# Kernel tuning notes

Hardware: AMD Instinct MI355X
Metric: run time of the kernel (lower is better)

## Reference

```python
import jax, jax.numpy as jnp
import numpy as np

B, T, N, H, D = 4, 512, 4, 8, 64
FACTOR = 5


def setup_inputs() -> dict:
    key = jax.random.key(0)
    k1, k2, k3, k4 = jax.random.split(key, 4)
    queries = jax.random.normal(k1, (B, T, N, H, D), dtype=jnp.float32)
    keys = jax.random.normal(k2, (B, T, N, H, D), dtype=jnp.float32)
    values = jax.random.normal(k3, (B, T, N, H, D), dtype=jnp.float32)
    sample_k = min(FACTOR * int(np.ceil(np.log(T))), T)  # = 35
    index_sample = jax.random.randint(k4, (T, sample_k), 0, T)
    return {"queries": queries, "keys": keys, "values": values,
            "index_sample": index_sample}


def _merge_heads(x):
    # [B, T, N, H, D] -> [B, H, T, N*D]  (matches transpose(3,2).reshape.transpose(2,1))
    b, t, n, h, d = x.shape
    return jnp.transpose(x, (0, 1, 3, 2, 4)).reshape(b, t, h, n * d).transpose(0, 2, 1, 3)


def reference(queries, keys, values, index_sample):
    b, t, n, h, d = queries.shape
    e = n * d
    Q = _merge_heads(queries)   # [B, H, T, E]
    K = _merge_heads(keys)
    V = _merge_heads(values)
    u = index_sample.shape[1]   # sample_k == n_top == factor*ceil(ln T)

    # --- _prob_QK: sampled QK scores, sparsity measure, top-u query select ---
    K_sample = K[:, :, index_sample, :]                      # [B, H, T, u, E]
    QK_sample = jnp.einsum('bhte,bhtse->bhts', Q, K_sample)  # [B, H, T, u]
    M = QK_sample.max(axis=-1) - QK_sample.sum(axis=-1) / t  # [B, H, T]
    _, M_top = jax.lax.top_k(M, u)                           # [B, H, u]
    Q_reduce = jnp.take_along_axis(Q, M_top[..., None], axis=2)  # [B, H, u, E]
    scores = jnp.einsum('bhue,bhte->bhut', Q_reduce, K)      # [B, H, u, T]

    # scale uses 1/sqrt(d_k) of the ORIGINAL query last dim (D), not N*D
    scores = scores * (1.0 / jnp.sqrt(jnp.asarray(d, scores.dtype)))

    # --- initial context (mask_flag=False): mean of V broadcast over T ---
    context = jnp.broadcast_to(V.mean(axis=2, keepdims=True), (b, h, t, e))

    # --- update context at selected query positions ---
    attn = jax.nn.softmax(scores, axis=-1)                   # [B, H, u, T]
    update = jnp.einsum('bhut,bhte->bhue', attn, V)          # [B, H, u, E]
    bi = jnp.arange(b)[:, None, None]
    hi = jnp.arange(h)[None, :, None]
    context = context.at[bi, hi, M_top].set(update)          # scatter-write

    # [B, H, T, E] -> [B, T, N, H, D]
    out = context.transpose(0, 2, 1, 3).reshape(b, t, h, n, d).transpose(0, 1, 3, 2, 4)
    return out
```

## Files before the change

### kernel.cpp

```cpp
#include <hip/hip_runtime.h>
#include <stdint.h>

#define BB 4
#define TT 512
#define NN 4
#define HH 8
#define DD 64
#define EE 256
#define ROWS 2048
#define UPAD 36
#define NCH 8
#define CH 64


__global__ __launch_bounds__(1024)
void vmean_kernel(const float* __restrict__ v, float* __restrict__ vmean) {
    __shared__ float part[4][EE];
    int bh = blockIdx.x;
    int b = bh >> 3, h = bh & 7;
    int e = threadIdx.x & 255;
    int chunk = threadIdx.x >> 8;
    int n = e >> 6, d = e & 63;
    size_t base = (size_t)b * TT * ROWS + (size_t)(n * HH + h) * DD + d;
    float acc = 0.f;
    int t0 = chunk * 128;
    for (int t = t0; t < t0 + 128; ++t)
        acc += v[base + (size_t)t * ROWS];
    part[chunk][e] = acc;
    __syncthreads();
    if (threadIdx.x < EE)
        vmean[bh * EE + threadIdx.x] =
            (part[0][threadIdx.x] + part[1][threadIdx.x] +
             part[2][threadIdx.x] + part[3][threadIdx.x]) * (1.0f / TT);
}

__global__ void fill_kernel(const float* __restrict__ vmean,
                            float* __restrict__ out) {
    size_t tid4 = ((size_t)blockIdx.x * 256 + threadIdx.x) << 2;
    int d = tid4 & 63;
    size_t rest = tid4 >> 6;
    int h = rest & 7;  rest >>= 3;
    int n = rest & 3;  rest >>= 2;
    int b = (int)(rest >> 9);
    int e = (n << 6) + d;
    int bh = (b << 3) + h;
    float4 val = *(const float4*)(vmean + (size_t)bh * EE + e);
    *(float4*)(out + tid4) = val;
}

__global__ void m_kernel(const float* __restrict__ q,
                         const float* __restrict__ k,
                         const int* __restrict__ idx,
                         float* __restrict__ M, int U) {
    int wave = threadIdx.x >> 6, lane = threadIdx.x & 63;
    int r = (blockIdx.x << 2) + wave;
    int t = r & (TT - 1);
    int bh = r >> 9;
    int b = bh >> 3, h = bh & 7;
    int g = lane >> 4, x = lane & 15;
    int n = x >> 2;
    int dbase = ((x & 3) << 4);
    size_t colbase = (size_t)(n * HH + h) * DD + dbase;
    size_t qrow = ((size_t)(b * TT + t)) * ROWS + colbase;
    float4 qv0 = *(const float4*)(q + qrow);
    float4 qv1 = *(const float4*)(q + qrow + 4);
    float4 qv2 = *(const float4*)(q + qrow + 8);
    float4 qv3 = *(const float4*)(q + qrow + 12);
    float mx = -3.4e38f, sm = 0.f;
    int NB = (U + 3) >> 2;
    for (int bs = 0; bs < NB; ++bs) {
        int s = (bs << 2) + g;
        int valid = s < U;
        int sc = valid ? s : (U - 1);
        int kt = idx[t * U + sc] & (TT - 1);
        size_t krow = ((size_t)(b * TT + kt)) * ROWS + colbase;
        float4 kv0 = *(const float4*)(k + krow);
        float4 kv1 = *(const float4*)(k + krow + 4);
        float4 kv2 = *(const float4*)(k + krow + 8);
        float4 kv3 = *(const float4*)(k + krow + 12);
        float dot = qv0.x * kv0.x + qv0.y * kv0.y + qv0.z * kv0.z + qv0.w * kv0.w
                  + qv1.x * kv1.x + qv1.y * kv1.y + qv1.z * kv1.z + qv1.w * kv1.w
                  + qv2.x * kv2.x + qv2.y * kv2.y + qv2.z * kv2.z + qv2.w * kv2.w
                  + qv3.x * kv3.x + qv3.y * kv3.y + qv3.z * kv3.z + qv3.w * kv3.w;
        #pragma unroll
        for (int off = 1; off < 16; off <<= 1)
            dot += __shfl_xor(dot, off, 64);
        if (valid) { mx = fmaxf(mx, dot); sm += dot; }
    }
    mx = fmaxf(mx, __shfl_xor(mx, 16, 64));
    mx = fmaxf(mx, __shfl_xor(mx, 32, 64));
    sm += __shfl_xor(sm, 16, 64);
    sm += __shfl_xor(sm, 32, 64);
    if (lane == 0) M[r] = mx - sm * (1.0f / TT);
}

__global__ void topk_kernel(const float* __restrict__ M,
                            int* __restrict__ Mtop, int U) {
    __shared__ float sM[TT];
    int bh = blockIdx.x;
    int t = threadIdx.x;
    sM[t] = M[bh * TT + t];
    if (t < 64) Mtop[bh * 64 + t] = 0;
    __syncthreads();
    float mv = sM[t];
    int rank = 0;
    for (int i = 0; i < TT; ++i) {
        float o = sM[i];
        rank += (o > mv) || (o == mv && i < t);
    }
    if (rank < U) Mtop[bh * 64 + rank] = t;
}

__global__ __launch_bounds__(256)
void attn_partial(const float* __restrict__ q, const float* __restrict__ k,
                  const float* __restrict__ v, const int* __restrict__ Mtop,
                  float* __restrict__ Opart, float* __restrict__ ml, int U) {
    __shared__ float qs[UPAD * 130];
    __shared__ float Bs[CH * 132];
    __shared__ float S[UPAD * 68];

    int bx = blockIdx.x;
    int bh = bx >> 3, ch = bx & 7;
    int b = bh >> 3, h = bh & 7;
    int tid = threadIdx.x;
    int wv = tid >> 6, l = tid & 63;

    float acc[4][4];
    #pragma unroll
    for (int i = 0; i < 4; ++i)
        #pragma unroll
        for (int j = 0; j < 4; ++j) acc[i][j] = 0.f;

    for (int h2 = 0; h2 < 2; ++h2) {
        int eb = h2 * 128;
        for (int u = wv; u < UPAD; u += 4) {
            int uu = (u < U) ? u : (U - 1);
            int qt = Mtop[bh * 64 + uu] & (TT - 1);
            size_t rowq = ((size_t)(b * TT + qt)) * ROWS;
            #pragma unroll
            for (int j = 0; j < 2; ++j) {
                int e = eb + l + 64 * j;
                qs[u * 130 + l + 64 * j] = q[rowq + (size_t)((e >> 6) * HH + h) * DD + (e & 63)];
            }
        }
        for (int r = wv; r < CH; r += 4) {
            size_t rowk = ((size_t)(b * TT + ch * CH + r)) * ROWS;
            #pragma unroll
            for (int j = 0; j < 2; ++j) {
                int e = eb + l + 64 * j;
                Bs[r * 129 + l + 64 * j] = k[rowk + (size_t)((e >> 6) * HH + h) * DD + (e & 63)];
            }
        }
        __syncthreads();
        if (tid < 144) {
            int ug = tid >> 4, tg = tid & 15;
            int u0 = ug << 2, t0 = tg << 2;
            for (int e = 0; e < 128; ++e) {
                float kx0 = Bs[(t0 + 0) * 129 + e];
                float kx1 = Bs[(t0 + 1) * 129 + e];
                float kx2 = Bs[(t0 + 2) * 129 + e];
                float kx3 = Bs[(t0 + 3) * 129 + e];
                #pragma unroll
                for (int i = 0; i < 4; ++i) {
                    float qv = qs[(u0 + i) * 130 + e];
                    acc[i][0] += qv * kx0;
                    acc[i][1] += qv * kx1;
                    acc[i][2] += qv * kx2;
                    acc[i][3] += qv * kx3;
                }
            }
        }
        __syncthreads();
    }
    if (tid < 144) {
        int ug = tid >> 4, tg = tid & 15;
        int u0 = ug << 2, t0 = tg << 2;
        #pragma unroll
        for (int i = 0; i < 4; ++i)
            #pragma unroll
            for (int j = 0; j < 4; ++j)
                S[(u0 + i) * 68 + t0 + j] = acc[i][j] * 0.125f;
    }
    __syncthreads();

    if (tid < UPAD) {
        float m = -3.4e38f;
        for (int t = 0; t < CH; ++t) m = fmaxf(m, S[tid * 68 + t]);
        float lsum = 0.f;
        for (int t = 0; t < CH; ++t) {
            float p = __expf(S[tid * 68 + t] - m);
            S[tid * 68 + t] = p;
            lsum += p;
        }
        size_t mli = ((size_t)(bh * NCH + ch) * UPAD + tid) * 2;
        ml[mli] = m;
        ml[mli + 1] = lsum;
    }
    __syncthreads();

    int ugp = tid >> 5, el = tid & 31;
    int u0p = ugp * 5;
    for (int vh = 0; vh < 2; ++vh) {
        for (int r = wv; r < CH; r += 4) {
            size_t rowv = ((size_t)(b * TT + ch * CH + r)) * ROWS;
            #pragma unroll
            for (int j = 0; j < 2; ++j) {
                int e = vh * 128 + l + 64 * j;
                Bs[r * 132 + l + 64 * j] = v[rowv + (size_t)((e >> 6) * HH + h) * DD + (e & 63)];
            }
        }
        __syncthreads();
        float4 o[5];
        #pragma unroll
        for (int i = 0; i < 5; ++i) o[i] = make_float4(0.f, 0.f, 0.f, 0.f);
        for (int t = 0; t < CH; ++t) {
            float4 v4 = *(const float4*)&Bs[t * 132 + 4 * el];
            #pragma unroll
            for (int i = 0; i < 5; ++i) {
                int uc = u0p + i; if (uc > 35) uc = 35;
                float p = S[uc * 68 + t];
                o[i].x += p * v4.x; o[i].y += p * v4.y;
                o[i].z += p * v4.z; o[i].w += p * v4.w;
            }
        }
        #pragma unroll
        for (int i = 0; i < 5; ++i) {
            int u = u0p + i;
            if (u < UPAD)
                *(float4*)&Opart[((size_t)(bh * NCH + ch) * UPAD + u) * EE + vh * 128 + 4 * el] = o[i];
        }
        __syncthreads();
    }
}

__global__ void combine_kernel(const float* __restrict__ Opart,
                               const float* __restrict__ ml,
                               const int* __restrict__ Mtop,
                               float* __restrict__ out, int U) {
    int bx = blockIdx.x;
    int bh = bx / U, ui = bx % U;
    int b = bh >> 3, h = bh & 7;
    int el = threadIdx.x;
    float mc[NCH], lc[NCH];
    float gm = -3.4e38f;
    #pragma unroll
    for (int c = 0; c < NCH; ++c) {
        size_t mli = ((size_t)(bh * NCH + c) * UPAD + ui) * 2;
        mc[c] = ml[mli]; lc[c] = ml[mli + 1];
        gm = fmaxf(gm, mc[c]);
    }
    float L = 0.f;
    float fc[NCH];
    #pragma unroll
    for (int c = 0; c < NCH; ++c) { fc[c] = __expf(mc[c] - gm); L += lc[c] * fc[c]; }
    float inv = 1.0f / L;
    float4 a = make_float4(0.f, 0.f, 0.f, 0.f);
    #pragma unroll
    for (int c = 0; c < NCH; ++c) {
        float4 o = *(const float4*)&Opart[((size_t)(bh * NCH + c) * UPAD + ui) * EE + 4 * el];
        a.x += fc[c] * o.x; a.y += fc[c] * o.y;
        a.z += fc[c] * o.z; a.w += fc[c] * o.w;
    }
    int qt = Mtop[bh * 64 + ui] & (TT - 1);
    int e0 = 4 * el, n = el >> 4;
    size_t ooff = ((size_t)(b * TT + qt)) * ROWS + (size_t)(n * HH + h) * DD + (e0 & 63);
    a.x *= inv; a.y *= inv; a.z *= inv; a.w *= inv;
    *(float4*)(out + ooff) = a;
}

__global__ void update_kernel(const float* __restrict__ q,
                              const float* __restrict__ k,
                              const float* __restrict__ v,
                              const int* __restrict__ Mtop,
                              float* __restrict__ out, int U) {
    __shared__ float qs[EE];
    __shared__ float sc[TT];
    __shared__ float red[256];
    int blk = blockIdx.x;
    int ui = blk % U;
    int bh = blk / U;
    int b = bh >> 3, h = bh & 7;
    int tid = threadIdx.x;
    int qt = Mtop[bh * 64 + ui] & (TT - 1);
    {
        int n = tid >> 6, d = tid & 63;
        qs[tid] = q[((size_t)(b * TT + qt)) * ROWS + (size_t)(n * HH + h) * DD + d];
    }
    __syncthreads();
    #pragma unroll
    for (int rep = 0; rep < 2; ++rep) {
        int t = tid + rep * 256;
        size_t kb = ((size_t)(b * TT + t)) * ROWS + (size_t)h * DD;
        float acc = 0.f;
        #pragma unroll
        for (int n = 0; n < NN; ++n) {
            const float* kn = k + kb + (size_t)n * HH * DD;
            #pragma unroll 4
            for (int d4 = 0; d4 < DD; d4 += 4) {
                float4 kv = *(const float4*)(kn + d4);
                int e = n * 64 + d4;
                acc += qs[e] * kv.x + qs[e + 1] * kv.y + qs[e + 2] * kv.z + qs[e + 3] * kv.w;
            }
        }
        sc[t] = acc * 0.125f;
    }
    __syncthreads();
    red[tid] = fmaxf(sc[tid], sc[tid + 256]);
    __syncthreads();
    for (int s = 128; s > 0; s >>= 1) {
        if (tid < s) red[tid] = fmaxf(red[tid], red[tid + s]);
        __syncthreads();
    }
    float mx = red[0];
    __syncthreads();
    float e0 = __expf(sc[tid] - mx);
    float e1 = __expf(sc[tid + 256] - mx);
    sc[tid] = e0; sc[tid + 256] = e1;
    red[tid] = e0 + e1;
    __syncthreads();
    for (int s = 128; s > 0; s >>= 1) {
        if (tid < s) red[tid] += red[tid + s];
        __syncthreads();
    }
    float inv = 1.0f / red[0];
    __syncthreads();
    {
        int n = tid >> 6, d = tid & 63;
        size_t vb = (size_t)b * TT * ROWS + (size_t)(n * HH + h) * DD + d;
        float acc = 0.f;
        for (int t = 0; t < TT; ++t)
            acc += sc[t] * v[vb + (size_t)t * ROWS];
        out[((size_t)(b * TT + qt)) * ROWS + (size_t)(n * HH + h) * DD + d] = acc * inv;
    }
}

__global__ __launch_bounds__(1024)
void fused_probattn(const float* __restrict__ qp, const float* __restrict__ kp,
                    const float* __restrict__ vp, const int* __restrict__ idx,
                    float* __restrict__ out, int U) {
    __shared__ float vmean[EE];
    __shared__ float M[TT];
    __shared__ float sc[TT];
    __shared__ float qs[EE];
    __shared__ float red[64];
    __shared__ int   Mtop[64];
    const int bh = blockIdx.x;
    const int b = bh >> 3, h = bh & 7;
    const int tid = threadIdx.x;
    const int wave = tid >> 6, lane = tid & 63;
    if (tid < EE) {
        int n = tid >> 6, d = tid & 63;
        size_t base = (size_t)b * TT * ROWS + (size_t)(n * HH + h) * DD + d;
        float acc = 0.f;
        for (int t = 0; t < TT; ++t) acc += vp[base + (size_t)t * ROWS];
        vmean[tid] = acc * (1.0f / TT);
    }
    __syncthreads();
    for (int i = tid; i < TT * EE; i += 1024) {
        int t = i >> 8, e = i & 255;
        int n = e >> 6, d = e & 63;
        out[((size_t)(b * TT + t)) * ROWS + (size_t)(n * HH + h) * DD + d] = vmean[e];
    }
    {
        int e = lane << 2;
        int n = e >> 6, d = e & 63;
        size_t ebase = (size_t)(n * HH + h) * DD + d;
        for (int t = wave; t < TT; t += 16) {
            float4 qv = *(const float4*)(qp + ((size_t)(b * TT + t)) * ROWS + ebase);
            float mx = -3.4e38f, sm = 0.f;
            for (int s = 0; s < U; ++s) {
                int kt = idx[t * U + s] & (TT - 1);
                float4 kv = *(const float4*)(kp + ((size_t)(b * TT + kt)) * ROWS + ebase);
                float dot = qv.x * kv.x + qv.y * kv.y + qv.z * kv.z + qv.w * kv.w;
                #pragma unroll
                for (int off = 32; off; off >>= 1) dot += __shfl_xor(dot, off, 64);
                mx = fmaxf(mx, dot);
                sm += dot;
            }
            if (lane == 0) M[t] = mx - sm * (1.0f / TT);
        }
    }
    __syncthreads();
    if (tid < 64) Mtop[tid] = 0;
    __syncthreads();
    if (tid < TT) {
        float mv = M[tid];
        int rank = 0;
        for (int i = 0; i < TT; ++i) {
            float o = M[i];
            rank += (o > mv) || (o == mv && i < tid);
        }
        if (rank < U) Mtop[rank] = tid;
    }
    __syncthreads();
    for (int ui = 0; ui < U; ++ui) {
        int qt = Mtop[ui];
        if (tid < EE) {
            int n = tid >> 6, d = tid & 63;
            qs[tid] = qp[((size_t)(b * TT + qt)) * ROWS + (size_t)(n * HH + h) * DD + d];
        }
        __syncthreads();
        if (tid < TT) {
            float acc = 0.f;
            size_t kb = ((size_t)(b * TT + tid)) * ROWS + (size_t)h * DD;
            for (int n = 0; n < NN; ++n) {
                const float* kn = kp + kb + (size_t)n * HH * DD;
                for (int d = 0; d < DD; ++d) acc += qs[n * 64 + d] * kn[d];
            }
            sc[tid] = acc * 0.125f;
        }
        __syncthreads();
        float val = (tid < TT) ? sc[tid] : -3.4e38f;
        #pragma unroll
        for (int off = 32; off; off >>= 1) val = fmaxf(val, __shfl_xor(val, off, 64));
        if (lane == 0) red[wave] = val;
        __syncthreads();
        if (tid == 0) {
            float m = red[0];
            for (int w = 1; w < 16; ++w) m = fmaxf(m, red[w]);
            red[32] = m;
        }
        __syncthreads();
        float mx = red[32];
        float ev = 0.f;
        if (tid < TT) { ev = __expf(sc[tid] - mx); sc[tid] = ev; }
        __syncthreads();
        float sv = ev;
        #pragma unroll
        for (int off = 32; off; off >>= 1) sv += __shfl_xor(sv, off, 64);
        if (lane == 0) red[wave] = sv;
        __syncthreads();
        if (tid == 0) {
            float s = 0.f;
            for (int w = 0; w < 16; ++w) s += red[w];
            red[32] = s;
        }
        __syncthreads();
        float inv = 1.0f / red[32];
        if (tid < EE) {
            int n = tid >> 6, d = tid & 63;
            size_t vb = (size_t)b * TT * ROWS + (size_t)(n * HH + h) * DD + d;
            float acc = 0.f;
            for (int t = 0; t < TT; ++t) acc += sc[t] * vp[vb + (size_t)t * ROWS];
            out[((size_t)(b * TT + qt)) * ROWS + (size_t)(n * HH + h) * DD + d] = acc * inv;
        }
        __syncthreads();
    }
}

extern "C" void kernel_launch(void* const* d_in, const int* in_sizes, int n_in,
                              void* d_out, int out_size, void* d_ws, size_t ws_size,
                              hipStream_t stream) {
    const float* q = (const float*)d_in[0];
    const float* k = (const float*)d_in[1];
    const float* v = (const float*)d_in[2];
    const int* idx = (const int*)d_in[3];
    float* out = (float*)d_out;
    int U = in_sizes[3] / TT;

    const size_t NEED_FLASH = 204800 + (size_t)32 * NCH * UPAD * EE * 4 + 1024;
    const size_t NEED_MID = 160 * 1024;
    char* ws = (char*)d_ws;
    float* M     = (float*)(ws);
    int*   Mtop  = (int*)  (ws + 65536);
    float* vmean = (float*)(ws + 98304);
    float* ml    = (float*)(ws + 131072);
    float* Opart = (float*)(ws + 204800);

    if (ws_size >= NEED_FLASH && U == 35) {
        vmean_kernel<<<BB * HH, 1024, 0, stream>>>(v, vmean);
        fill_kernel<<<4096, 256, 0, stream>>>(vmean, out);
        m_kernel<<<BB * HH * TT / 4, 256, 0, stream>>>(q, k, idx, M, U);
        topk_kernel<<<BB * HH, TT, 0, stream>>>(M, Mtop, U);
        attn_partial<<<BB * HH * NCH, 256, 0, stream>>>(q, k, v, Mtop, Opart, ml, U);
        combine_kernel<<<BB * HH * U, 64, 0, stream>>>(Opart, ml, Mtop, out, U);
    } else if (ws_size >= NEED_MID) {
        vmean_kernel<<<BB * HH, 1024, 0, stream>>>(v, vmean);
        fill_kernel<<<4096, 256, 0, stream>>>(vmean, out);
        m_kernel<<<BB * HH * TT / 4, 256, 0, stream>>>(q, k, idx, M, U);
        topk_kernel<<<BB * HH, TT, 0, stream>>>(M, Mtop, U);
        update_kernel<<<BB * HH * U, 256, 0, stream>>>(q, k, v, Mtop, out, U);
    } else {
        fused_probattn<<<BB * HH, 1024, 0, stream>>>(q, k, v, idx, out, U);
    }
}
```

Before: 195.0 us.

## Split V-mean into partial blocks, fold reduction into top-k, remap m_kernel blocks for XCD locality

The V mean is now computed by 256 small blocks writing partial sums instead of 32 large 1024-thread blocks, which spreads the V read across more CUs. The final reduction of those partials moves into the top-k kernel, and the fill kernel is launched after top-k. m_kernel's block index is remapped so that each XCD handles a fixed set of (b,h) pairs, aiming to improve L2 reuse of K rows. vpart shares workspace with Opart, which is safe only because the partials are consumed before attn_partial writes Opart.

```diff
diff --git a/kernel.cpp b/kernel.cpp
--- a/kernel.cpp
+++ b/kernel.cpp
@@ -13,25 +13,20 @@
 #define CH 64
 
 
-__global__ __launch_bounds__(1024)
-void vmean_kernel(const float* __restrict__ v, float* __restrict__ vmean) {
-    __shared__ float part[4][EE];
-    int bh = blockIdx.x;
+__global__ void vmean_part_kernel(const float* __restrict__ v,
+                                  float* __restrict__ vpart) {
+    int blk = blockIdx.x;
+    int chunk = blk & 7;
+    int bh = blk >> 3;
     int b = bh >> 3, h = bh & 7;
-    int e = threadIdx.x & 255;
-    int chunk = threadIdx.x >> 8;
+    int e = threadIdx.x;
     int n = e >> 6, d = e & 63;
     size_t base = (size_t)b * TT * ROWS + (size_t)(n * HH + h) * DD + d;
     float acc = 0.f;
-    int t0 = chunk * 128;
-    for (int t = t0; t < t0 + 128; ++t)
+    int t0 = chunk * 64;
+    for (int t = t0; t < t0 + 64; ++t)
         acc += v[base + (size_t)t * ROWS];
-    part[chunk][e] = acc;
-    __syncthreads();
-    if (threadIdx.x < EE)
-        vmean[bh * EE + threadIdx.x] =
-            (part[0][threadIdx.x] + part[1][threadIdx.x] +
-             part[2][threadIdx.x] + part[3][threadIdx.x]) * (1.0f / TT);
+    vpart[blk * EE + e] = acc;
 }
 
 __global__ void fill_kernel(const float* __restrict__ vmean,
@@ -53,9 +48,10 @@
                          const int* __restrict__ idx,
                          float* __restrict__ M, int U) {
     int wave = threadIdx.x >> 6, lane = threadIdx.x & 63;
-    int r = (blockIdx.x << 2) + wave;
-    int t = r & (TT - 1);
-    int bh = r >> 9;
+    int xcd = blockIdx.x & 7;
+    int bh = (xcd << 2) | ((blockIdx.x >> 3) & 3);
+    int t = ((blockIdx.x >> 5) << 2) + wave;
+    int r = (bh << 9) + t;
     int b = bh >> 3, h = bh & 7;
     int g = lane >> 4, x = lane & 15;
     int n = x >> 2;
@@ -95,12 +91,21 @@
 }
 
 __global__ void topk_kernel(const float* __restrict__ M,
-                            int* __restrict__ Mtop, int U) {
+                            int* __restrict__ Mtop,
+                            const float* __restrict__ vpart,
+                            float* __restrict__ vmean, int U) {
     __shared__ float sM[TT];
     int bh = blockIdx.x;
     int t = threadIdx.x;
     sM[t] = M[bh * TT + t];
     if (t < 64) Mtop[bh * 64 + t] = 0;
+    if (t < EE) {
+        float acc = 0.f;
+        #pragma unroll
+        for (int c = 0; c < 8; ++c)
+            acc += vpart[(bh * 8 + c) * EE + t];
+        vmean[bh * EE + t] = acc * (1.0f / TT);
+    }
     __syncthreads();
     float mv = sM[t];
     int rank = 0;
@@ -266,6 +271,45 @@
     size_t ooff = ((size_t)(b * TT + qt)) * ROWS + (size_t)(n * HH + h) * DD + (e0 & 63);
     a.x *= inv; a.y *= inv; a.z *= inv; a.w *= inv;
     *(float4*)(out + ooff) = a;
+}
+
+
+__global__ __launch_bounds__(1024)
+void vmean_kernel(const float* __restrict__ v, float* __restrict__ vmean) {
+    __shared__ float part[4][EE];
+    int bh = blockIdx.x;
+    int b = bh >> 3, h = bh & 7;
+    int e = threadIdx.x & 255;
+    int chunk = threadIdx.x >> 8;
+    int n = e >> 6, d = e & 63;
+    size_t base = (size_t)b * TT * ROWS + (size_t)(n * HH + h) * DD + d;
+    float acc = 0.f;
+    int t0 = chunk * 128;
+    for (int t = t0; t < t0 + 128; ++t)
+        acc += v[base + (size_t)t * ROWS];
+    part[chunk][e] = acc;
+    __syncthreads();
+    if (threadIdx.x < EE)
+        vmean[bh * EE + threadIdx.x] =
+            (part[0][threadIdx.x] + part[1][threadIdx.x] +
+             part[2][threadIdx.x] + part[3][threadIdx.x]) * (1.0f / TT);
+}
+
+__global__ void topk_only_kernel(const float* __restrict__ M,
+                                 int* __restrict__ Mtop, int U) {
+    __shared__ float sM[TT];
+    int bh = blockIdx.x;
+    int t = threadIdx.x;
+    sM[t] = M[bh * TT + t];
+    if (t < 64) Mtop[bh * 64 + t] = 0;
+    __syncthreads();
+    float mv = sM[t];
+    int rank = 0;
+    for (int i = 0; i < TT; ++i) {
+        float o = sM[i];
+        rank += (o > mv) || (o == mv && i < t);
+    }
+    if (rank < U) Mtop[bh * 64 + rank] = t;
 }
 
 __global__ void update_kernel(const float* __restrict__ q,
@@ -466,19 +510,20 @@
     float* vmean = (float*)(ws + 98304);
     float* ml    = (float*)(ws + 131072);
     float* Opart = (float*)(ws + 204800);
+    float* vpart = (float*)(ws + 204800);
 
     if (ws_size >= NEED_FLASH && U == 35) {
-        vmean_kernel<<<BB * HH, 1024, 0, stream>>>(v, vmean);
+        vmean_part_kernel<<<BB * HH * 8, 256, 0, stream>>>(v, vpart);
+        m_kernel<<<BB * HH * TT / 4, 256, 0, stream>>>(q, k, idx, M, U);
+        topk_kernel<<<BB * HH, TT, 0, stream>>>(M, Mtop, vpart, vmean, U);
         fill_kernel<<<4096, 256, 0, stream>>>(vmean, out);
-        m_kernel<<<BB * HH * TT / 4, 256, 0, stream>>>(q, k, idx, M, U);
-        topk_kernel<<<BB * HH, TT, 0, stream>>>(M, Mtop, U);
         attn_partial<<<BB * HH * NCH, 256, 0, stream>>>(q, k, v, Mtop, Opart, ml, U);
         combine_kernel<<<BB * HH * U, 64, 0, stream>>>(Opart, ml, Mtop, out, U);
     } else if (ws_size >= NEED_MID) {
         vmean_kernel<<<BB * HH, 1024, 0, stream>>>(v, vmean);
         fill_kernel<<<4096, 256, 0, stream>>>(vmean, out);
         m_kernel<<<BB * HH * TT / 4, 256, 0, stream>>>(q, k, idx, M, U);
-        topk_kernel<<<BB * HH, TT, 0, stream>>>(M, Mtop, U);
+        topk_only_kernel<<<BB * HH, TT, 0, stream>>>(M, Mtop, U);
         update_kernel<<<BB * HH * U, 256, 0, stream>>>(q, k, v, Mtop, out, U);
     } else {
         fused_probattn<<<BB * HH, 1024, 0, stream>>>(q, k, v, idx, out, U);
```

New measurement: 186.8 us. 1.04x faster.
